# Kernel optimization log

Hardware: AMD Instinct MI355X
Metric: run time of the kernel (lower is better)

The kernel has to match this reference:

```python
import jax, jax.numpy as jnp
import numpy as np

B, T, P, E, H, VP2, L, V = 64, 32, 64, 512, 512, 16, 16, 30000
IN = E + VP2 + L + H + E  # 1568 = LSTMCell input width


def setup_inputs() -> dict:
    key = jax.random.key(0)
    ks = list(jax.random.split(key, 24))
    it = iter(ks)
    n = lambda shape, s: jax.random.normal(next(it), shape, jnp.float32) * s
    return {
        "image": n((B, P, E), 1.0),
        "view_position": n((B, VP2), 1.0),
        "label": jax.random.uniform(next(it), (B, L), jnp.float32),
        "topic": n((B, E), 1.0),
        "temp": jnp.ones((B, 1), jnp.float32),
        "text": jax.random.randint(next(it), (B, T), 0, V),
        "word_emb": n((V, E), 0.05),
        "fc_v_w": n((H, E), 0.05), "fc_v_b": jnp.zeros((H,), jnp.float32),
        "fc_h_w": n((H, E), 0.05), "fc_h_b": jnp.zeros((H,), jnp.float32),
        "fc_m_w": n((H, E), 0.05), "fc_m_b": jnp.zeros((H,), jnp.float32),
        "w_ih": n((4 * H, IN), 0.02), "w_hh": n((4 * H, H), 0.02),
        "b_ih": jnp.zeros((4 * H,), jnp.float32), "b_hh": jnp.zeros((4 * H,), jnp.float32),
        "fc_w": n((2 * E, H), 0.05), "fc_b": jnp.zeros((2 * E,), jnp.float32),
        "fc_hh_w": n((H, E), 0.05), "fc_hh_b": jnp.zeros((H,), jnp.float32),
        "fc_s_w": n((H, E), 0.05), "fc_s_b": jnp.zeros((H,), jnp.float32),
        "fc_z_w": n((1, H), 0.05), "fc_z_b": jnp.zeros((1,), jnp.float32),
        "fc_p_w": n((V, E), 0.05), "fc_p_b": jnp.zeros((V,), jnp.float32),
    }


def reference(image, view_position, label, topic, temp, word_emb,
              fc_v_w, fc_v_b, fc_h_w, fc_h_b, fc_m_w, fc_m_b,
              w_ih, w_hh, b_ih, b_hh, fc_w, fc_b,
              fc_hh_w, fc_hh_b, fc_s_w, fc_s_b, fc_z_w, fc_z_b,
              fc_p_w, fc_p_b, text):
    # Init (dropout=0 / eval mode)
    image_mean = image.mean(1)                                   # [B,E]
    v = jnp.einsum('bpe,he->bph', image, fc_v_w) + fc_v_b        # [B,P,H]
    h0 = jnp.tanh(image_mean @ fc_h_w.T + fc_h_b)                # [B,H]
    m0 = jnp.tanh(image_mean @ fc_m_w.T + fc_m_b)                # [B,H]

    # teacher forcing ratio = 1.0: input token at step t is text[:, t-1], BOS (=0) at t=0
    bos = jnp.zeros((B, 1), text.dtype)
    toks = jnp.concatenate([bos, text[:, :-1]], axis=1).T        # [T,B]

    def step(carry, tok):
        h, m = carry
        emb = word_emb[tok]                                      # [B,E]
        x = jnp.concatenate([image_mean, view_position, label, topic, emb], axis=1)
        gates = x @ w_ih.T + b_ih + h @ w_hh.T + b_hh            # [B,4H]
        i, f, g, o = jnp.split(gates, 4, axis=1)                 # torch LSTMCell gate order
        m_new = jax.nn.sigmoid(f) * m + jax.nn.sigmoid(i) * jnp.tanh(g)
        h_new = jax.nn.sigmoid(o) * jnp.tanh(m_new)
        hs = jax.nn.relu(h_new @ fc_w.T + fc_b)                  # [B,2E]
        hh, s = hs[:, :E], hs[:, E:]
        _hh = hh @ fc_hh_w.T + fc_hh_b                           # [B,H]
        _s = s @ fc_s_w.T + fc_s_b                               # [B,H]
        ext = jnp.concatenate([v, _s[:, None, :]], axis=1)       # [B,P+1,H]
        z = jnp.tanh(ext + _hh[:, None, :])
        z = jnp.einsum('bph,h->bp', z, fc_z_w[0]) + fc_z_b[0]    # [B,P+1]
        a = jax.nn.softmax(z, axis=1)                            # attention weights
        feats = jnp.concatenate([image, s[:, None, :]], axis=1)  # [B,P+1,E]
        c = jnp.einsum('bp,bpe->be', a, feats)                   # context [B,E]
        logit = ((c + hh) @ fc_p_w.T + fc_p_b) / temp            # [B,V]
        logp = jax.nn.log_softmax(logit, axis=1)
        return (h_new, m_new), (a, logp)

    _, (attn, logp) = jax.lax.scan(step, (h0, m0), toks)
    logp_bt = logp.transpose(1, 0, 2)                            # [B,T,V]
    attn_bt = attn.transpose(1, 0, 2)                            # [B,T,P+1]
    # __sample_text=False -> _text = argmax; log_prob(argmax) = max log prob
    sum_log_prob = jnp.max(logp, axis=2).sum(0)                  # [B]
    return logp_bt, attn_bt, sum_log_prob
```

## Files before the change

kernel.cpp:

```cpp
#include <hip/hip_runtime.h>


typedef unsigned short bf16u;
typedef __attribute__((ext_vector_type(8))) short short8;
typedef __attribute__((ext_vector_type(4))) float floatx4;

#define DEV __device__ __forceinline__

DEV float b2f(bf16u u) { return __uint_as_float(((unsigned)u) << 16); }
DEV bf16u f2b(float f) {
  unsigned u = __float_as_uint(f);
  u = (u + 0x7fffu + ((u >> 16) & 1u)) >> 16;
  return (bf16u)u;
}

DEV float ftanh(float x) {
  float e = __expf(2.0f * x);
  float r = __builtin_amdgcn_rcpf(e + 1.0f);
  return __builtin_fmaf(-2.0f, r, 1.0f);
}
DEV float fsigm(float x) {
  return __builtin_amdgcn_rcpf(1.0f + __expf(-x));
}

__global__ __launch_bounds__(256)
void cvt_kernel(const float* __restrict__ src, bf16u* __restrict__ dst, int n)
{
  int i = blockIdx.x * 256 + threadIdx.x;
  if (i < n) dst[i] = f2b(src[i]);
}

__global__ __launch_bounds__(256)
void mean_kernel(const float* __restrict__ image, float* __restrict__ imean)
{
  int b = blockIdx.x;
  for (int e = threadIdx.x; e < 512; e += 256) {
    float s = 0.f;
    for (int p = 0; p < 64; ++p) s += image[(size_t)(b * 64 + p) * 512 + e];
    imean[b * 512 + e] = s * (1.0f / 64.0f);
  }
}

__global__ __launch_bounds__(256)
void prep_kernel(const float* __restrict__ imean, const float* __restrict__ vp,
                 const float* __restrict__ lab, const float* __restrict__ topic,
                 const int* __restrict__ text, const float* __restrict__ wemb,
                 bf16u* __restrict__ X)
{
  int b = blockIdx.x;
  for (int t = 0; t < 32; ++t) {
    bf16u* xr = X + ((size_t)t * 64 + b) * 1568;
    int tok = (t == 0) ? 0 : text[b * 32 + t - 1];
    for (int e = threadIdx.x; e < 512; e += 256) {
      xr[e] = f2b(imean[b * 512 + e]);
      xr[544 + e] = f2b(topic[b * 512 + e]);
      xr[1056 + e] = f2b(wemb[(size_t)tok * 512 + e]);
    }
    if (threadIdx.x < 16) {
      xr[512 + threadIdx.x] = f2b(vp[b * 16 + threadIdx.x]);
      xr[528 + threadIdx.x] = f2b(lab[b * 16 + threadIdx.x]);
    }
  }
}

__global__ __launch_bounds__(256)
void pack_whh(const float* __restrict__ whh, bf16u* __restrict__ wpack)
{
  int idx = blockIdx.x * 256 + threadIdx.x;
  int gr = idx >> 9, k = idx & 511;
  int gate = gr >> 9, win = gr & 511;
  int blk = win >> 4, lc = win & 15;
  int rr = gate * 16 + lc;
  wpack[(size_t)blk * 32768 + (((k >> 3) * 64 + rr) << 3) + (k & 7)] =
      f2b(whh[(size_t)gr * 512 + k]);
}

#define BK 32
#define LDT 40

template<int MODE>
__global__ __launch_bounds__(256)
void gemm_bt(const bf16u* __restrict__ A, int lda,
             const bf16u* __restrict__ W, int ldw,
             const float* __restrict__ bias1, const float* __restrict__ bias2,
             bf16u* __restrict__ C, int ldc,
             int M, int N, int K, int act,
             const float* __restrict__ temp,
             float* __restrict__ outbase,
             float* __restrict__ pmax, float* __restrict__ psum)
{
  __shared__ __align__(16) bf16u As[128 * LDT];
  __shared__ __align__(16) bf16u Ws[128 * LDT];
  const int tid = threadIdx.x;
  const int n0 = blockIdx.x * 128;
  const int m0 = blockIdx.y * 128;
  const int wave = tid >> 6, lane = tid & 63;
  const int wm = wave >> 1, wn = wave & 1;
  const int q = lane >> 4, l16 = lane & 15;
  const int r0 = tid >> 2, s0 = tid & 3;

  const floatx4 zero = {0.f, 0.f, 0.f, 0.f};
  floatx4 acc[4][4];
#pragma unroll
  for (int i = 0; i < 4; ++i)
#pragma unroll
    for (int j = 0; j < 4; ++j) acc[i][j] = zero;

  int ar0 = m0 + r0;      if (ar0 >= M) ar0 = M - 1;
  int ar1 = m0 + r0 + 64; if (ar1 >= M) ar1 = M - 1;
  int wr0 = n0 + r0;      if (wr0 >= N) wr0 = N - 1;
  int wr1 = n0 + r0 + 64; if (wr1 >= N) wr1 = N - 1;
  const bf16u* Ap0 = A + (size_t)ar0 * lda + s0 * 8;
  const bf16u* Ap1 = A + (size_t)ar1 * lda + s0 * 8;
  const bf16u* Wp0 = W + (size_t)wr0 * ldw + s0 * 8;
  const bf16u* Wp1 = W + (size_t)wr1 * ldw + s0 * 8;

  for (int k0 = 0; k0 < K; k0 += BK) {
    const int4 a0 = *(const int4*)(Ap0 + k0);
    const int4 a1 = *(const int4*)(Ap1 + k0);
    const int4 w0 = *(const int4*)(Wp0 + k0);
    const int4 w1 = *(const int4*)(Wp1 + k0);
    __syncthreads();
    *(int4*)(As + r0 * LDT + s0 * 8) = a0;
    *(int4*)(As + (r0 + 64) * LDT + s0 * 8) = a1;
    *(int4*)(Ws + r0 * LDT + s0 * 8) = w0;
    *(int4*)(Ws + (r0 + 64) * LDT + s0 * 8) = w1;
    __syncthreads();
    short8 af[4], wf[4];
#pragma unroll
    for (int i = 0; i < 4; ++i) {
      af[i] = *(const short8*)(As + (wm * 64 + i * 16 + l16) * LDT + q * 8);
      wf[i] = *(const short8*)(Ws + (wn * 64 + i * 16 + l16) * LDT + q * 8);
    }
#pragma unroll
    for (int i = 0; i < 4; ++i)
#pragma unroll
      for (int j = 0; j < 4; ++j)
        acc[i][j] = __builtin_amdgcn_mfma_f32_16x16x32_bf16(af[i], wf[j], acc[i][j], 0, 0, 0);
  }

  int colb[4]; float bias[4];
#pragma unroll
  for (int j = 0; j < 4; ++j) {
    int col = n0 + wn * 64 + j * 16 + l16;
    colb[j] = col;
    int cc = col < N ? col : N - 1;
    float bv = 0.f;
    if (bias1) bv += bias1[cc];
    if (bias2) bv += bias2[cc];
    bias[j] = bv;
  }

  if (MODE == 2) {
#pragma unroll
    for (int i = 0; i < 4; ++i) {
#pragma unroll
      for (int r = 0; r < 4; ++r) {
        int row = m0 + wm * 64 + i * 16 + q * 4 + r;
        if (row < M) {
#pragma unroll
          for (int j = 0; j < 4; ++j) {
            int col = colb[j];
            if (col < N) {
              float v = acc[i][j][r] + bias[j];
              if (act == 1) v = fmaxf(v, 0.f);
              C[(size_t)row * ldc + col] = f2b(v);
            }
          }
        }
      }
    }
  } else {
    int pc = blockIdx.x * 2 + wn;
#pragma unroll
    for (int i = 0; i < 4; ++i) {
#pragma unroll
      for (int r = 0; r < 4; ++r) {
        int row = m0 + wm * 64 + i * 16 + q * 4 + r;
        int bb = row & 63, tt = row >> 6;
        float rt = 1.0f / temp[bb];
        float vals[4];
#pragma unroll
        for (int j = 0; j < 4; ++j) {
          int col = colb[j];
          float v = (acc[i][j][r] + bias[j]) * rt;
          if (col < N) {
            outbase[(size_t)bb * 960000 + (size_t)tt * 30000 + col] = v;
            vals[j] = v;
          } else vals[j] = -1e30f;
        }
        float mx = fmaxf(fmaxf(vals[0], vals[1]), fmaxf(vals[2], vals[3]));
#pragma unroll
        for (int off = 1; off < 16; off <<= 1) mx = fmaxf(mx, __shfl_xor(mx, off));
        float s = 0.f;
#pragma unroll
        for (int j = 0; j < 4; ++j)
          s += (vals[j] > -1e29f) ? __expf(vals[j] - mx) : 0.f;
#pragma unroll
        for (int off = 1; off < 16; off <<= 1) s += __shfl_xor(s, off);
        if (l16 == 0) {
          pmax[(size_t)row * 470 + pc] = mx;
          psum[(size_t)row * 470 + pc] = s;
        }
      }
    }
  }
}

template<int ROWS>
__global__ void gemm_tmpl(const float* __restrict__ A, int lda,
                          const float* __restrict__ W, int ldw,
                          const float* __restrict__ bias1,
                          float* __restrict__ C, int ldc,
                          int M, int N, int K, int act)
{
  constexpr int RP = ROWS + 4;
  extern __shared__ __align__(16) float Ash[];
  const int tid = threadIdx.x;
  const int m0 = blockIdx.y * ROWS;
  const int n0 = blockIdx.x * 256;
  for (int idx = tid; idx < ROWS * K; idx += 256) {
    int r = idx / K, k = idx - r * K;
    int rr = m0 + r; if (rr >= M) rr = M - 1;
    Ash[k * RP + r] = A[(size_t)rr * lda + k];
  }
  __syncthreads();
  int n = n0 + tid;
  if (n >= N) return;
  float acc[ROWS];
#pragma unroll
  for (int r = 0; r < ROWS; ++r) acc[r] = 0.f;
  const float* wr = W + (size_t)n * ldw;
  for (int k = 0; k < K; ++k) {
    float w = wr[k];
    const float* a = Ash + (size_t)k * RP;
#pragma unroll
    for (int r = 0; r < ROWS; ++r) acc[r] += w * a[r];
  }
  float bv = bias1 ? bias1[n] : 0.f;
#pragma unroll
  for (int r = 0; r < ROWS; ++r) {
    int row = m0 + r;
    if (row < M) {
      float v = acc[r] + bv;
      if (act == 1) v = fmaxf(v, 0.f);
      else if (act == 2) v = tanhf(v);
      C[(size_t)row * ldc + n] = v;
    }
  }
}

__global__ __launch_bounds__(256)
void init_state(const float* __restrict__ h0b, const float* __restrict__ m0b,
                bf16u* __restrict__ hOut, float* __restrict__ mbuf)
{
  int i = blockIdx.x * 256 + threadIdx.x;
  int b = i >> 9, jj = i & 511;
  hOut[(((jj >> 3) * 64 + b) << 3) + (jj & 7)] = f2b(h0b[i]);
  mbuf[i] = m0b[i];
}

__global__ __launch_bounds__(256)
void lstm_step(const bf16u* __restrict__ wpack, const bf16u* __restrict__ gx,
               const bf16u* __restrict__ hIn, bf16u* __restrict__ hOut,
               float* __restrict__ mbuf, bf16u* __restrict__ h_all, int t)
{
  extern __shared__ __align__(16) char smem[];
  bf16u* hsh = (bf16u*)smem;
  bf16u* wsh = (bf16u*)(smem + 65536);
  float* gsh = (float*)(smem + 131072);
  const int blk = blockIdx.x, tid = threadIdx.x;

  const int4* hsrc = (const int4*)hIn;
  const int4* wsrc = (const int4*)(wpack + (size_t)blk * 32768);
  int4* hdst = (int4*)hsh; int4* wdst = (int4*)wsh;
#pragma unroll
  for (int u = 0; u < 16; ++u) {
    hdst[tid + 256 * u] = hsrc[tid + 256 * u];
    wdst[tid + 256 * u] = wsrc[tid + 256 * u];
  }
  __syncthreads();

  const int wave = tid >> 6, lane = tid & 63;
  const int wm = wave >> 1, wn = wave & 1, q = lane >> 4, l16 = lane & 15;
  const floatx4 zero = {0.f, 0.f, 0.f, 0.f};
  floatx4 acc[2][2];
#pragma unroll
  for (int i = 0; i < 2; ++i)
#pragma unroll
    for (int j = 0; j < 2; ++j) acc[i][j] = zero;

  for (int s = 0; s < 16; ++s) {
    short8 af[2], wf[2];
#pragma unroll
    for (int i = 0; i < 2; ++i)
      af[i] = *(const short8*)(hsh + ((((s * 4 + q) * 64) + wm * 32 + i * 16 + l16) << 3));
#pragma unroll
    for (int j = 0; j < 2; ++j)
      wf[j] = *(const short8*)(wsh + ((((s * 4 + q) * 64) + wn * 32 + j * 16 + l16) << 3));
#pragma unroll
    for (int i = 0; i < 2; ++i)
#pragma unroll
      for (int j = 0; j < 2; ++j)
        acc[i][j] = __builtin_amdgcn_mfma_f32_16x16x32_bf16(af[i], wf[j], acc[i][j], 0, 0, 0);
  }
#pragma unroll
  for (int i = 0; i < 2; ++i)
#pragma unroll
    for (int j = 0; j < 2; ++j)
#pragma unroll
      for (int r = 0; r < 4; ++r)
        gsh[(wn * 32 + j * 16 + l16) * 65 + (wm * 32 + i * 16 + q * 4 + r)] = acc[i][j][r];
  __syncthreads();

#pragma unroll
  for (int u = 0; u < 4; ++u) {
    int p = tid + 256 * u;
    int b = p >> 4, lc = p & 15;
    int jj = blk * 16 + lc;
    const bf16u* gxr = gx + ((size_t)t * 64 + b) * 2048;
    float ai = gsh[(lc) * 65 + b]        + b2f(gxr[jj]);
    float af = gsh[(16 + lc) * 65 + b]   + b2f(gxr[512 + jj]);
    float ag = gsh[(32 + lc) * 65 + b]   + b2f(gxr[1024 + jj]);
    float ao = gsh[(48 + lc) * 65 + b]   + b2f(gxr[1536 + jj]);
    float iv = fsigm(ai);
    float fv = fsigm(af);
    float gv = ftanh(ag);
    float ov = fsigm(ao);
    float mm = fv * mbuf[b * 512 + jj] + iv * gv;
    float hn = ov * ftanh(mm);
    mbuf[b * 512 + jj] = mm;
    bf16u hb = f2b(hn);
    hOut[(((jj >> 3) * 64 + b) << 3) + (jj & 7)] = hb;
    h_all[((size_t)t * 64 + b) * 512 + jj] = hb;
  }
}

__global__ __launch_bounds__(256)
void attn_kernel(const bf16u* __restrict__ vbuf, const float* __restrict__ image,
                 const bf16u* __restrict__ hs_bf, const bf16u* __restrict__ hh2,
                 const bf16u* __restrict__ s2, const float* __restrict__ wz,
                 const float* __restrict__ zb, float* __restrict__ attn_out,
                 bf16u* __restrict__ ctx)
{
  const int rown = blockIdx.x;
  const int bb = rown & 63, tt = rown >> 6;
  const int tid = threadIdx.x;
  const int wave = tid >> 6, lane = tid & 63;

  __shared__ float2 hwz[512];
  __shared__ float zpart[64][4];
  __shared__ float spart[4];
  __shared__ float ash[66];
  __shared__ float4 cpart[128];

  float sv0, sv1;
  {
    unsigned hr = *(const unsigned*)(hh2 + (size_t)rown * 512 + tid * 2);
    unsigned sr = *(const unsigned*)(s2 + (size_t)rown * 512 + tid * 2);
    float2 w2 = *(const float2*)(wz + tid * 2);
    hwz[tid * 2]     = make_float2(b2f((bf16u)(hr & 0xffffu)), w2.x);
    hwz[tid * 2 + 1] = make_float2(b2f((bf16u)(hr >> 16)), w2.y);
    sv0 = b2f((bf16u)(sr & 0xffffu));
    sv1 = b2f((bf16u)(sr >> 16));
  }
  __syncthreads();

  {
    const bf16u* vrow = vbuf + (size_t)(bb * 64 + lane) * 512 + wave * 128;
    float acc = 0.f;
    for (int c = 0; c < 16; ++c) {
      short8 vv = *(const short8*)(vrow + c * 8);
#pragma unroll
      for (int e = 0; e < 8; ++e) {
        float2 hz = hwz[wave * 128 + c * 8 + e];
        float tn = ftanh(b2f((bf16u)vv[e]) + hz.x);
        acc = __builtin_fmaf(tn, hz.y, acc);
      }
    }
    zpart[lane][wave] = acc;
  }

  {
    float2 h0 = hwz[tid * 2], h1 = hwz[tid * 2 + 1];
    float sacc = ftanh(sv0 + h0.x) * h0.y + ftanh(sv1 + h1.x) * h1.y;
#pragma unroll
    for (int off = 1; off < 64; off <<= 1) sacc += __shfl_xor(sacc, off);
    if (lane == 0) spart[wave] = sacc;
  }
  __syncthreads();

  if (wave == 0) {
    float zbv = zb[0];
    float4 zp = *(const float4*)zpart[lane];
    float z = zp.x + zp.y + zp.z + zp.w + zbv;
    float zs = spart[0] + spart[1] + spart[2] + spart[3] + zbv;
    float m = fmaxf(z, zs);
#pragma unroll
    for (int off = 1; off < 64; off <<= 1) m = fmaxf(m, __shfl_xor(m, off));
    float ez = __expf(z - m);
    float es = __expf(zs - m);
    float ssum = ez + (lane == 0 ? es : 0.f);
#pragma unroll
    for (int off = 1; off < 64; off <<= 1) ssum += __shfl_xor(ssum, off);
    float inv = 1.0f / ssum;
    ash[lane] = ez * inv;
    if (lane == 0) ash[64] = es * inv;
  }
  __syncthreads();

  size_t aoff = (size_t)bb * 2080 + (size_t)tt * 65;
  if (tid < 65) attn_out[aoff + tid] = ash[tid];

  const int e4 = tid & 127;
  const int ph = tid >> 7;
  float4 cacc = {0.f, 0.f, 0.f, 0.f};
  const float* img = image + ((size_t)bb * 64 + (size_t)ph * 32) * 512 + e4 * 4;
  for (int p = 0; p < 32; ++p) {
    float a = ash[ph * 32 + p];
    float4 iv = *(const float4*)(img + (size_t)p * 512);
    cacc.x = __builtin_fmaf(a, iv.x, cacc.x);
    cacc.y = __builtin_fmaf(a, iv.y, cacc.y);
    cacc.z = __builtin_fmaf(a, iv.z, cacc.z);
    cacc.w = __builtin_fmaf(a, iv.w, cacc.w);
  }
  if (ph == 1) cpart[e4] = cacc;
  __syncthreads();
  if (ph == 0) {
    float4 o = cpart[e4];
    cacc.x += o.x; cacc.y += o.y; cacc.z += o.z; cacc.w += o.w;
    const bf16u* hsrow = hs_bf + (size_t)rown * 1024;
    int2 hraw = *(const int2*)(hsrow + e4 * 4);
    int2 sraw = *(const int2*)(hsrow + 512 + e4 * 4);
    float a64 = ash[64];
    cacc.x += a64 * b2f((bf16u)(sraw.x & 0xffff)) + b2f((bf16u)(hraw.x & 0xffff));
    cacc.y += a64 * b2f((bf16u)((unsigned)sraw.x >> 16)) + b2f((bf16u)((unsigned)hraw.x >> 16));
    cacc.z += a64 * b2f((bf16u)(sraw.y & 0xffff)) + b2f((bf16u)(hraw.y & 0xffff));
    cacc.w += a64 * b2f((bf16u)((unsigned)sraw.y >> 16)) + b2f((bf16u)((unsigned)hraw.y >> 16));
    unsigned o0 = (unsigned)f2b(cacc.x) | ((unsigned)f2b(cacc.y) << 16);
    unsigned o1 = (unsigned)f2b(cacc.z) | ((unsigned)f2b(cacc.w) << 16);
    *(int2*)(ctx + (size_t)rown * 512 + e4 * 4) = make_int2((int)o0, (int)o1);
  }
}

__global__ __launch_bounds__(256)
void reduce_lse(const float* __restrict__ pmax, const float* __restrict__ psum,
                float* __restrict__ lse, float* __restrict__ rmax)
{
  int row = blockIdx.x * 4 + (threadIdx.x >> 6);
  int lane = threadIdx.x & 63;
  const float* pm = pmax + (size_t)row * 470;
  const float* ps = psum + (size_t)row * 470;
  float m = -1e30f, s = 0.f;
  for (int c = lane; c < 470; c += 64) {
    float mi = pm[c];
    float si = ps[c];
    if (mi > m) { s = s * __expf(m - mi) + si; m = mi; }
    else        { s += si * __expf(mi - m); }
  }
#pragma unroll
  for (int off = 1; off < 64; off <<= 1) {
    float mo = __shfl_xor(m, off);
    float so = __shfl_xor(s, off);
    float mn = fmaxf(m, mo);
    s = s * __expf(m - mn) + so * __expf(mo - mn);
    m = mn;
  }
  if (lane == 0) {
    rmax[row] = m;
    lse[row] = m + logf(s);
  }
}

__global__ __launch_bounds__(256)
void finalize_kernel(float* __restrict__ out, const float* __restrict__ lse)
{
  int idx = blockIdx.x * 256 + threadIdx.x;
  if (idx >= 15360000) return;
  int rflat = idx / 7500;
  int c4 = idx - rflat * 7500;
  float L = lse[(rflat & 31) * 64 + (rflat >> 5)];
  float4* p = (float4*)(out + (size_t)rflat * 30000 + (size_t)c4 * 4);
  float4 v = *p;
  v.x -= L; v.y -= L; v.z -= L; v.w -= L;
  *p = v;
}

__global__ void slp_kernel(const float* __restrict__ rmax,
                           const float* __restrict__ lse, float* __restrict__ out)
{
  int b = threadIdx.x;
  float s = 0.f;
  for (int t = 0; t < 32; ++t) { int r = t * 64 + b; s += rmax[r] - lse[r]; }
  out[61440000 + 133120 + b] = s;
}

extern "C" void kernel_launch(void* const* d_in, const int* in_sizes, int n_in,
                              void* d_out, int out_size, void* d_ws, size_t ws_size,
                              hipStream_t stream)
{
  const float* image   = (const float*)d_in[0];
  const float* vp      = (const float*)d_in[1];
  const float* lab     = (const float*)d_in[2];
  const float* topic   = (const float*)d_in[3];
  const float* temp    = (const float*)d_in[4];
  const int*   text    = (const int*)d_in[5];
  const float* wemb    = (const float*)d_in[6];
  const float* fc_v_w  = (const float*)d_in[7];
  const float* fc_v_b  = (const float*)d_in[8];
  const float* fc_h_w  = (const float*)d_in[9];
  const float* fc_h_b  = (const float*)d_in[10];
  const float* fc_m_w  = (const float*)d_in[11];
  const float* fc_m_b  = (const float*)d_in[12];
  const float* w_ih    = (const float*)d_in[13];
  const float* w_hh    = (const float*)d_in[14];
  const float* b_ih    = (const float*)d_in[15];
  const float* b_hh    = (const float*)d_in[16];
  const float* fc_w    = (const float*)d_in[17];
  const float* fc_b    = (const float*)d_in[18];
  const float* fc_hh_w = (const float*)d_in[19];
  const float* fc_hh_b = (const float*)d_in[20];
  const float* fc_s_w  = (const float*)d_in[21];
  const float* fc_s_b  = (const float*)d_in[22];
  const float* fc_z_w  = (const float*)d_in[23];
  const float* fc_z_b  = (const float*)d_in[24];
  const float* fc_p_w  = (const float*)d_in[25];
  const float* fc_p_b  = (const float*)d_in[26];
  float* out = (float*)d_out;

  char* base = (char*)d_ws;
  size_t off = 0;
  auto alloc = [&](size_t bytes) -> char* {
    char* p = base + off;
    off += (bytes + 255) & ~(size_t)255;
    return p;
  };
  bf16u* X       = (bf16u*)alloc(2048ull * 1568 * 2);
  bf16u* w_ih_bf = (bf16u*)alloc(2048ull * 1568 * 2);
  bf16u* gx_bf   = (bf16u*)alloc(2048ull * 2048 * 2);
  bf16u* image_bf= (bf16u*)alloc(4096ull * 512 * 2);
  bf16u* wpackb  = (bf16u*)alloc(2048ull * 512 * 2);
  bf16u* fcv_bf  = (bf16u*)alloc(512ull * 512 * 2);
  bf16u* fcw_bf  = (bf16u*)alloc(1024ull * 512 * 2);
  bf16u* fchh_bf = (bf16u*)alloc(512ull * 512 * 2);
  bf16u* fcs_bf  = (bf16u*)alloc(512ull * 512 * 2);
  bf16u* fcp_bf  = (bf16u*)alloc(30000ull * 512 * 2);
  float* imean   = (float*)alloc(64ull * 512 * 4);
  float* h0b     = (float*)alloc(64ull * 512 * 4);
  float* m0b     = (float*)alloc(64ull * 512 * 4);
  bf16u* vbuf    = (bf16u*)alloc(4096ull * 512 * 2);
  bf16u* hA      = (bf16u*)alloc(64ull * 512 * 2);
  bf16u* hB      = (bf16u*)alloc(64ull * 512 * 2);
  float* mbuf    = (float*)alloc(64ull * 512 * 4);
  bf16u* h_all   = (bf16u*)alloc(2048ull * 512 * 2);
  float* rmaxb   = (float*)alloc(2048ull * 4);
  float* lseb    = (float*)alloc(2048ull * 4);
  bf16u* hs_bf   = (bf16u*)w_ih_bf;
  bf16u* ctx     = (bf16u*)(w_ih_bf + 2048ull * 1024);
  bf16u* hhbuf   = (bf16u*)X;
  bf16u* sbuf    = (bf16u*)(X + 2048ull * 512);
  float* pmaxb   = (float*)gx_bf;
  float* psumb   = (float*)(gx_bf + 2048ull * 2048);
  (void)in_sizes; (void)n_in; (void)out_size; (void)ws_size;

  mean_kernel<<<64, 256, 0, stream>>>(image, imean);
  prep_kernel<<<64, 256, 0, stream>>>(imean, vp, lab, topic, text, wemb, X);
  cvt_kernel<<<12544, 256, 0, stream>>>(w_ih, w_ih_bf, 2048 * 1568);
  cvt_kernel<<<8192, 256, 0, stream>>>(image, image_bf, 4096 * 512);
  cvt_kernel<<<1024, 256, 0, stream>>>(fc_v_w, fcv_bf, 512 * 512);
  cvt_kernel<<<2048, 256, 0, stream>>>(fc_w, fcw_bf, 1024 * 512);
  cvt_kernel<<<1024, 256, 0, stream>>>(fc_hh_w, fchh_bf, 512 * 512);
  cvt_kernel<<<1024, 256, 0, stream>>>(fc_s_w, fcs_bf, 512 * 512);
  cvt_kernel<<<60000, 256, 0, stream>>>(fc_p_w, fcp_bf, 30000 * 512);
  pack_whh<<<4096, 256, 0, stream>>>(w_hh, wpackb);

  gemm_bt<2><<<dim3(16, 16), 256, 0, stream>>>(X, 1568, w_ih_bf, 1568, b_ih, b_hh,
      gx_bf, 2048, 2048, 2048, 1568, 0, nullptr, nullptr, nullptr, nullptr);
  gemm_bt<2><<<dim3(4, 32), 256, 0, stream>>>(image_bf, 512, fcv_bf, 512, fc_v_b, nullptr,
      vbuf, 512, 4096, 512, 512, 0, nullptr, nullptr, nullptr, nullptr);
  gemm_tmpl<32><<<dim3(2, 2), 256, 512 * 36 * 4, stream>>>(
      imean, 512, fc_h_w, 512, fc_h_b, h0b, 512, 64, 512, 512, 2);
  gemm_tmpl<32><<<dim3(2, 2), 256, 512 * 36 * 4, stream>>>(
      imean, 512, fc_m_w, 512, fc_m_b, m0b, 512, 64, 512, 512, 2);

  init_state<<<128, 256, 0, stream>>>(h0b, m0b, hA, mbuf);
  const int lstm_lds = 65536 + 65536 + 64 * 65 * 4;
  for (int t = 0; t < 32; ++t) {
    const bf16u* hi = (t & 1) ? hB : hA;
    bf16u* ho = (t & 1) ? hA : hB;
    lstm_step<<<32, 256, lstm_lds, stream>>>(wpackb, gx_bf, hi, ho, mbuf, h_all, t);
  }

  gemm_bt<2><<<dim3(8, 16), 256, 0, stream>>>(h_all, 512, fcw_bf, 512, fc_b, nullptr,
      hs_bf, 1024, 2048, 1024, 512, 1, nullptr, nullptr, nullptr, nullptr);
  gemm_bt<2><<<dim3(4, 16), 256, 0, stream>>>(hs_bf, 1024, fchh_bf, 512, fc_hh_b, nullptr,
      hhbuf, 512, 2048, 512, 512, 0, nullptr, nullptr, nullptr, nullptr);
  gemm_bt<2><<<dim3(4, 16), 256, 0, stream>>>(hs_bf + 512, 1024, fcs_bf, 512, fc_s_b, nullptr,
      sbuf, 512, 2048, 512, 512, 0, nullptr, nullptr, nullptr, nullptr);

  attn_kernel<<<2048, 256, 0, stream>>>(vbuf, image, hs_bf, hhbuf, sbuf,
      fc_z_w, fc_z_b, out + 61440000, ctx);

  gemm_bt<1><<<dim3(235, 16), 256, 0, stream>>>(ctx, 512, fcp_bf, 512, fc_p_b, nullptr,
      nullptr, 0, 2048, 30000, 512, 0, temp, out, pmaxb, psumb);

  reduce_lse<<<512, 256, 0, stream>>>(pmaxb, psumb, lseb, rmaxb);
  finalize_kernel<<<60000, 256, 0, stream>>>(out, lseb);
  slp_kernel<<<1, 64, 0, stream>>>(rmaxb, lseb, out);
}
```

Measured before the change: 1.189 ms.

## Fuse LSTM timesteps into persistent kernel with grid barrier; XCD-aware vocab GEMM tiling

Replaces 32 per-step LSTM launches with one persistent 32-block kernel that keeps W_hh slices resident in LDS, holds the cell state in registers, and synchronises steps with a global atomic barrier. This removes per-step launch overhead and repeated weight reloads. Separately, the vocab-projection GEMM switches to a 1D grid whose block index is remapped so that consecutive N tiles sharing the same weight rows land on the same XCD, improving L2 reuse. The grid barrier relies on all 32 blocks being co-resident.

```diff
diff --git a/kernel.cpp b/kernel.cpp
--- a/kernel.cpp
+++ b/kernel.cpp
@@ -92,8 +92,18 @@
   __shared__ __align__(16) bf16u As[128 * LDT];
   __shared__ __align__(16) bf16u Ws[128 * LDT];
   const int tid = threadIdx.x;
-  const int n0 = blockIdx.x * 128;
-  const int m0 = blockIdx.y * 128;
+  int m0, n0, ntile = 0;
+  if (MODE == 1) {
+    int p = blockIdx.x;
+    int xcd = p & 7, slot = p >> 3;
+    int nt, mt;
+    if (slot < 464) { nt = (slot >> 4) * 8 + xcd; mt = slot & 15; }
+    else { int idx = (slot - 464) * 8 + xcd; nt = 232 + (idx >> 4); mt = idx & 15; }
+    m0 = mt * 128; n0 = nt * 128; ntile = nt;
+  } else {
+    n0 = blockIdx.x * 128;
+    m0 = blockIdx.y * 128;
+  }
   const int wave = tid >> 6, lane = tid & 63;
   const int wm = wave >> 1, wn = wave & 1;
   const int q = lane >> 4, l16 = lane & 15;
@@ -171,7 +181,7 @@
       }
     }
   } else {
-    int pc = blockIdx.x * 2 + wn;
+    int pc = ntile * 2 + wn;
 #pragma unroll
     for (int i = 0; i < 4; ++i) {
 #pragma unroll
@@ -251,88 +261,128 @@
 }
 
 __global__ __launch_bounds__(256)
-void init_state(const float* __restrict__ h0b, const float* __restrict__ m0b,
-                bf16u* __restrict__ hOut, float* __restrict__ mbuf)
+void init_state(const float* __restrict__ h0b, bf16u* __restrict__ hOut,
+                unsigned* __restrict__ bar)
 {
   int i = blockIdx.x * 256 + threadIdx.x;
   int b = i >> 9, jj = i & 511;
   hOut[(((jj >> 3) * 64 + b) << 3) + (jj & 7)] = f2b(h0b[i]);
-  mbuf[i] = m0b[i];
-}
-
-__global__ __launch_bounds__(256)
-void lstm_step(const bf16u* __restrict__ wpack, const bf16u* __restrict__ gx,
-               const bf16u* __restrict__ hIn, bf16u* __restrict__ hOut,
-               float* __restrict__ mbuf, bf16u* __restrict__ h_all, int t)
+  if (i < 2)
+    __hip_atomic_store(bar + i, 0u, __ATOMIC_RELAXED, __HIP_MEMORY_SCOPE_AGENT);
+}
+
+DEV void gbar(unsigned* bar, int tid)
+{
+  __syncthreads();
+  if (tid == 0) {
+    __threadfence();
+    unsigned gen = __hip_atomic_load(bar + 1, __ATOMIC_RELAXED, __HIP_MEMORY_SCOPE_AGENT);
+    unsigned prev = __hip_atomic_fetch_add(bar, 1u, __ATOMIC_ACQ_REL, __HIP_MEMORY_SCOPE_AGENT);
+    if (prev == 31u) {
+      __hip_atomic_store(bar, 0u, __ATOMIC_RELAXED, __HIP_MEMORY_SCOPE_AGENT);
+      __hip_atomic_fetch_add(bar + 1, 1u, __ATOMIC_RELEASE, __HIP_MEMORY_SCOPE_AGENT);
+    } else {
+      while (__hip_atomic_load(bar + 1, __ATOMIC_ACQUIRE, __HIP_MEMORY_SCOPE_AGENT) == gen)
+        __builtin_amdgcn_s_sleep(2);
+    }
+    __threadfence();
+  }
+  __syncthreads();
+}
+
+__global__ __launch_bounds__(256)
+void lstm_all(const bf16u* __restrict__ wpack, const bf16u* __restrict__ gx,
+              bf16u* __restrict__ hA, bf16u* __restrict__ hB,
+              const float* __restrict__ m0b, bf16u* __restrict__ h_all,
+              unsigned* __restrict__ bar)
 {
   extern __shared__ __align__(16) char smem[];
-  bf16u* hsh = (bf16u*)smem;
-  bf16u* wsh = (bf16u*)(smem + 65536);
+  bf16u* wsh = (bf16u*)smem;
+  bf16u* hsh = (bf16u*)(smem + 65536);
   float* gsh = (float*)(smem + 131072);
   const int blk = blockIdx.x, tid = threadIdx.x;
 
-  const int4* hsrc = (const int4*)hIn;
-  const int4* wsrc = (const int4*)(wpack + (size_t)blk * 32768);
-  int4* hdst = (int4*)hsh; int4* wdst = (int4*)wsh;
-#pragma unroll
-  for (int u = 0; u < 16; ++u) {
-    hdst[tid + 256 * u] = hsrc[tid + 256 * u];
-    wdst[tid + 256 * u] = wsrc[tid + 256 * u];
-  }
-  __syncthreads();
+  {
+    const int4* wsrc = (const int4*)(wpack + (size_t)blk * 32768);
+    int4* wdst = (int4*)wsh;
+#pragma unroll
+    for (int u = 0; u < 16; ++u) wdst[tid + 256 * u] = wsrc[tid + 256 * u];
+  }
+
+  float mreg[4];
+#pragma unroll
+  for (int u = 0; u < 4; ++u) {
+    int p = tid + 256 * u;
+    mreg[u] = m0b[(p >> 4) * 512 + blk * 16 + (p & 15)];
+  }
 
   const int wave = tid >> 6, lane = tid & 63;
   const int wm = wave >> 1, wn = wave & 1, q = lane >> 4, l16 = lane & 15;
   const floatx4 zero = {0.f, 0.f, 0.f, 0.f};
-  floatx4 acc[2][2];
-#pragma unroll
-  for (int i = 0; i < 2; ++i)
-#pragma unroll
-    for (int j = 0; j < 2; ++j) acc[i][j] = zero;
-
-  for (int s = 0; s < 16; ++s) {
-    short8 af[2], wf[2];
+
+  for (int t = 0; t < 32; ++t) {
+    const bf16u* hIn = (t & 1) ? hB : hA;
+    bf16u* hOut = (t & 1) ? hA : hB;
+
+    {
+      const int4* hsrc = (const int4*)hIn;
+      int4* hdst = (int4*)hsh;
+#pragma unroll
+      for (int u = 0; u < 16; ++u) hdst[tid + 256 * u] = hsrc[tid + 256 * u];
+    }
+    __syncthreads();
+
+    floatx4 acc[2][2];
 #pragma unroll
     for (int i = 0; i < 2; ++i)
-      af[i] = *(const short8*)(hsh + ((((s * 4 + q) * 64) + wm * 32 + i * 16 + l16) << 3));
-#pragma unroll
-    for (int j = 0; j < 2; ++j)
-      wf[j] = *(const short8*)(wsh + ((((s * 4 + q) * 64) + wn * 32 + j * 16 + l16) << 3));
+#pragma unroll
+      for (int j = 0; j < 2; ++j) acc[i][j] = zero;
+
+    for (int s = 0; s < 16; ++s) {
+      short8 af[2], wf[2];
+#pragma unroll
+      for (int i = 0; i < 2; ++i)
+        af[i] = *(const short8*)(hsh + ((((s * 4 + q) * 64) + wm * 32 + i * 16 + l16) << 3));
+#pragma unroll
+      for (int j = 0; j < 2; ++j)
+        wf[j] = *(const short8*)(wsh + ((((s * 4 + q) * 64) + wn * 32 + j * 16 + l16) << 3));
+#pragma unroll
+      for (int i = 0; i < 2; ++i)
+#pragma unroll
+        for (int j = 0; j < 2; ++j)
+          acc[i][j] = __builtin_amdgcn_mfma_f32_16x16x32_bf16(af[i], wf[j], acc[i][j], 0, 0, 0);
+    }
 #pragma unroll
     for (int i = 0; i < 2; ++i)
 #pragma unroll
       for (int j = 0; j < 2; ++j)
-        acc[i][j] = __builtin_amdgcn_mfma_f32_16x16x32_bf16(af[i], wf[j], acc[i][j], 0, 0, 0);
-  }
-#pragma unroll
-  for (int i = 0; i < 2; ++i)
-#pragma unroll
-    for (int j = 0; j < 2; ++j)
-#pragma unroll
-      for (int r = 0; r < 4; ++r)
-        gsh[(wn * 32 + j * 16 + l16) * 65 + (wm * 32 + i * 16 + q * 4 + r)] = acc[i][j][r];
-  __syncthreads();
-
-#pragma unroll
-  for (int u = 0; u < 4; ++u) {
-    int p = tid + 256 * u;
-    int b = p >> 4, lc = p & 15;
-    int jj = blk * 16 + lc;
-    const bf16u* gxr = gx + ((size_t)t * 64 + b) * 2048;
-    float ai = gsh[(lc) * 65 + b]        + b2f(gxr[jj]);
-    float af = gsh[(16 + lc) * 65 + b]   + b2f(gxr[512 + jj]);
-    float ag = gsh[(32 + lc) * 65 + b]   + b2f(gxr[1024 + jj]);
-    float ao = gsh[(48 + lc) * 65 + b]   + b2f(gxr[1536 + jj]);
-    float iv = fsigm(ai);
-    float fv = fsigm(af);
-    float gv = ftanh(ag);
-    float ov = fsigm(ao);
-    float mm = fv * mbuf[b * 512 + jj] + iv * gv;
-    float hn = ov * ftanh(mm);
-    mbuf[b * 512 + jj] = mm;
-    bf16u hb = f2b(hn);
-    hOut[(((jj >> 3) * 64 + b) << 3) + (jj & 7)] = hb;
-    h_all[((size_t)t * 64 + b) * 512 + jj] = hb;
+#pragma unroll
+        for (int r = 0; r < 4; ++r)
+          gsh[(wn * 32 + j * 16 + l16) * 65 + (wm * 32 + i * 16 + q * 4 + r)] = acc[i][j][r];
+    __syncthreads();
+
+#pragma unroll
+    for (int u = 0; u < 4; ++u) {
+      int p = tid + 256 * u;
+      int b = p >> 4, lc = p & 15;
+      int jj = blk * 16 + lc;
+      const bf16u* gxr = gx + ((size_t)t * 64 + b) * 2048;
+      float ai = gsh[(lc) * 65 + b]        + b2f(gxr[jj]);
+      float af = gsh[(16 + lc) * 65 + b]   + b2f(gxr[512 + jj]);
+      float ag = gsh[(32 + lc) * 65 + b]   + b2f(gxr[1024 + jj]);
+      float ao = gsh[(48 + lc) * 65 + b]   + b2f(gxr[1536 + jj]);
+      float iv = fsigm(ai);
+      float fv = fsigm(af);
+      float gv = ftanh(ag);
+      float ov = fsigm(ao);
+      float mm = fv * mreg[u] + iv * gv;
+      float hn = ov * ftanh(mm);
+      mreg[u] = mm;
+      bf16u hb = f2b(hn);
+      hOut[(((jj >> 3) * 64 + b) << 3) + (jj & 7)] = hb;
+      h_all[((size_t)t * 64 + b) * 512 + jj] = hb;
+    }
+    gbar(bar, tid);
   }
 }
 
@@ -551,7 +601,7 @@
   bf16u* vbuf    = (bf16u*)alloc(4096ull * 512 * 2);
   bf16u* hA      = (bf16u*)alloc(64ull * 512 * 2);
   bf16u* hB      = (bf16u*)alloc(64ull * 512 * 2);
-  float* mbuf    = (float*)alloc(64ull * 512 * 4);
+  unsigned* barb = (unsigned*)alloc(256);
   bf16u* h_all   = (bf16u*)alloc(2048ull * 512 * 2);
   float* rmaxb   = (float*)alloc(2048ull * 4);
   float* lseb    = (float*)alloc(2048ull * 4);
@@ -583,13 +633,9 @@
   gemm_tmpl<32><<<dim3(2, 2), 256, 512 * 36 * 4, stream>>>(
       imean, 512, fc_m_w, 512, fc_m_b, m0b, 512, 64, 512, 512, 2);
 
-  init_state<<<128, 256, 0, stream>>>(h0b, m0b, hA, mbuf);
+  init_state<<<128, 256, 0, stream>>>(h0b, hA, barb);
   const int lstm_lds = 65536 + 65536 + 64 * 65 * 4;
-  for (int t = 0; t < 32; ++t) {
-    const bf16u* hi = (t & 1) ? hB : hA;
-    bf16u* ho = (t & 1) ? hA : hB;
-    lstm_step<<<32, 256, lstm_lds, stream>>>(wpackb, gx_bf, hi, ho, mbuf, h_all, t);
-  }
+  lstm_all<<<32, 256, lstm_lds, stream>>>(wpackb, gx_bf, hA, hB, m0b, h_all, barb);
 
   gemm_bt<2><<<dim3(8, 16), 256, 0, stream>>>(h_all, 512, fcw_bf, 512, fc_b, nullptr,
       hs_bf, 1024, 2048, 1024, 512, 1, nullptr, nullptr, nullptr, nullptr);
@@ -601,7 +647,7 @@
   attn_kernel<<<2048, 256, 0, stream>>>(vbuf, image, hs_bf, hhbuf, sbuf,
       fc_z_w, fc_z_b, out + 61440000, ctx);
 
-  gemm_bt<1><<<dim3(235, 16), 256, 0, stream>>>(ctx, 512, fcp_bf, 512, fc_p_b, nullptr,
+  gemm_bt<1><<<dim3(3760), 256, 0, stream>>>(ctx, 512, fcp_bf, 512, fc_p_b, nullptr,
       nullptr, 0, 2048, 30000, 512, 0, temp, out, pmaxb, psumb);
 
   reduce_lse<<<512, 256, 0, stream>>>(pmaxb, psumb, lseb, rmaxb);
```

Result: slower. 1.295 ms (+8.9%).
